# Performance work log

Measured on AMD Instinct MI355X. Metric: run time of the kernel, lower is better.

The kernel has to match this reference:

```python
import jax, jax.numpy as jnp
import numpy as np

HIDDEN = 2048
HEADS = 16
HEAD_DIM = HIDDEN // HEADS


def setup_inputs() -> dict:
    key = jax.random.key(0)
    ks = jax.random.split(key, 9)
    s = 1.0 / np.sqrt(HIDDEN)
    return {
        "hidden_states": jax.random.normal(ks[0], (2, 2048, HIDDEN), dtype=jnp.float32),
        "wq": jax.random.uniform(ks[1], (HIDDEN, HIDDEN), jnp.float32, -s, s),
        "bq": jax.random.uniform(ks[2], (HIDDEN,), jnp.float32, -s, s),
        "wk": jax.random.uniform(ks[3], (HIDDEN, HIDDEN), jnp.float32, -s, s),
        "bk": jax.random.uniform(ks[4], (HIDDEN,), jnp.float32, -s, s),
        "wv": jax.random.uniform(ks[5], (HIDDEN, HIDDEN), jnp.float32, -s, s),
        "bv": jax.random.uniform(ks[6], (HIDDEN,), jnp.float32, -s, s),
        "wo": jax.random.uniform(ks[7], (HIDDEN, HIDDEN), jnp.float32, -s, s),
        "bo": jax.random.uniform(ks[8], (HIDDEN,), jnp.float32, -s, s),
    }


def reference(hidden_states, wq, bq, wk, bk, wv, bv, wo, bo):
    B, S, _ = hidden_states.shape
    # QKV projections (nn.Linear: x @ W^T + b)
    q = hidden_states @ wq.T + bq
    k = hidden_states @ wk.T + bk
    v = hidden_states @ wv.T + bv
    # [B, S, H, D] -> [B, H, S, D]
    q = q.reshape(B, S, HEADS, HEAD_DIM).transpose(0, 2, 1, 3)
    k = k.reshape(B, S, HEADS, HEAD_DIM).transpose(0, 2, 1, 3)
    v = v.reshape(B, S, HEADS, HEAD_DIM).transpose(0, 2, 1, 3)
    scale = HEAD_DIM ** (-0.5)
    scores = jnp.einsum("bhqd,bhkd->bhqk", q, k) * scale  # [B,H,S,S]
    attn = jax.nn.softmax(scores, axis=-1)
    out = jnp.einsum("bhqk,bhkd->bhqd", attn, v)
    out = out.transpose(0, 2, 1, 3).reshape(B, S, HIDDEN)
    return out @ wo.T + bo
```

## Files before the change

### kernel.cpp

```cpp
#include <hip/hip_runtime.h>
#include <math.h>

#define HID 2048
#define NB  2
#define SEQ 2048
#define NT  (NB*SEQ)
#define NH  16
#define HD  128

typedef __attribute__((ext_vector_type(8))) _Float16 f16x8;
typedef __attribute__((ext_vector_type(4))) float    f32x4;

#define QSCALE 0.12751742f

__device__ __forceinline__ unsigned short f2h(float x) {
    union { _Float16 h; unsigned short u; } c;
    c.h = (_Float16)x;
    return c.u;
}

extern "C" __global__ __launch_bounds__(256)
void cast_x(const float* __restrict__ src, unsigned short* __restrict__ dst, int n4)
{
    const int i = blockIdx.x * 256 + threadIdx.x;
    if (i >= n4) return;
    const float4 x = ((const float4*)src)[i];
    ushort4 h;
    h.x = f2h(x.x); h.y = f2h(x.y); h.z = f2h(x.z); h.w = f2h(x.w);
    ((ushort4*)dst)[i] = h;
}

extern "C" __global__ __launch_bounds__(256)
void cast_w4(const float* __restrict__ s0, const float* __restrict__ s1,
             const float* __restrict__ s2, const float* __restrict__ s3,
             unsigned short* __restrict__ d0, unsigned short* __restrict__ d1,
             unsigned short* __restrict__ d2, unsigned short* __restrict__ d3,
             int n4)
{
    const int which = blockIdx.y;
    const float* __restrict__ src =
        (which==0) ? s0 : (which==1) ? s1 : (which==2) ? s2 : s3;
    unsigned short* __restrict__ dst =
        (which==0) ? d0 : (which==1) ? d1 : (which==2) ? d2 : d3;
    const int i = blockIdx.x * 256 + threadIdx.x;
    if (i >= n4) return;
    const float4 x = ((const float4*)src)[i];
    ushort4 h;
    h.x = f2h(x.x); h.y = f2h(x.y); h.z = f2h(x.z); h.w = f2h(x.w);
    ((ushort4*)dst)[i] = h;
}

extern "C" __global__ __launch_bounds__(256)
void qkv_f16(const unsigned short* __restrict__ Xh,
             const unsigned short* __restrict__ Wqh,
             const unsigned short* __restrict__ Wkh,
             const unsigned short* __restrict__ Wvh,
             const float* __restrict__ bq, const float* __restrict__ bk,
             const float* __restrict__ bv,
             unsigned short* __restrict__ Qb, unsigned short* __restrict__ Kb,
             unsigned short* __restrict__ Vb)
{
    const int on0 = blockIdx.x * 128;
    const int tm0 = blockIdx.y * 128;
    const int which = blockIdx.z;
    const unsigned short* __restrict__ W = (which==0) ? Wqh : (which==1) ? Wkh : Wvh;
    const float* __restrict__ bias      = (which==0) ? bq  : (which==1) ? bk  : bv;

    __shared__ unsigned short Ah[8192], Bh[8192];

    const int tid  = threadIdx.x;
    const int lane = tid & 63;
    const int w    = tid >> 6;
    const int wm   = (w & 1) * 64;
    const int wn   = (w >> 1) * 64;
    const int fr   = lane & 15;
    const int quad = lane >> 4;

    f32x4 acc[4][4];
    #pragma unroll
    for (int i = 0; i < 4; ++i)
        #pragma unroll
        for (int j = 0; j < 4; ++j)
            acc[i][j] = (f32x4){0.f, 0.f, 0.f, 0.f};

    for (int kb = 0; kb < HID/64; ++kb) {
        __syncthreads();
        const unsigned short* Asrc = Xh + (size_t)tm0*HID + kb*64;
        const unsigned short* Bsrc = W  + (size_t)on0*HID + kb*64;
        #pragma unroll
        for (int r = 0; r < 4; ++r) {
            const int p   = (r*4 + w)*64 + lane;
            const int row = p >> 3;
            const int c   = (p & 7) ^ (row & 7);
            __builtin_amdgcn_global_load_lds(
                (const __attribute__((address_space(1))) void*)(Asrc + (size_t)row*HID + c*8),
                (__attribute__((address_space(3))) void*)(Ah + (r*4 + w)*512), 16, 0, 0);
            __builtin_amdgcn_global_load_lds(
                (const __attribute__((address_space(1))) void*)(Bsrc + (size_t)row*HID + c*8),
                (__attribute__((address_space(3))) void*)(Bh + (r*4 + w)*512), 16, 0, 0);
        }
        __syncthreads();

        #pragma unroll
        for (int kk = 0; kk < 2; ++kk) {
            f16x8 a[4], b[4];
            #pragma unroll
            for (int i = 0; i < 4; ++i) {
                const int ra = wm + i*16 + fr;
                a[i] = *(const f16x8*)(Ah + (ra*8 + ((kk*4 + quad) ^ (ra & 7)))*8);
                const int rb = wn + i*16 + fr;
                b[i] = *(const f16x8*)(Bh + (rb*8 + ((kk*4 + quad) ^ (rb & 7)))*8);
            }
            #pragma unroll
            for (int i = 0; i < 4; ++i)
                #pragma unroll
                for (int j = 0; j < 4; ++j)
                    acc[i][j] = __builtin_amdgcn_mfma_f32_16x16x32_f16(a[i], b[j], acc[i][j], 0, 0, 0);
        }
    }

    const int col_l = fr;
    if (which == 2) {
        #pragma unroll
        for (int j = 0; j < 4; ++j) {
            const int o = on0 + wn + j*16 + col_l;
            const float bb = bias[o];
            const int h = o >> 7, d = o & (HD-1);
            #pragma unroll
            for (int i = 0; i < 4; ++i)
                #pragma unroll
                for (int rg = 0; rg < 4; ++rg) {
                    const int t = tm0 + wm + i*16 + quad*4 + rg;
                    const int b = t >> 11, s = t & (SEQ-1);
                    const int pos = (s & ~63) | (((s & 15) << 2) | ((s >> 4) & 3));
                    Vb[((size_t)(b*NH + h)*HD + d)*SEQ + pos] = f2h(acc[i][j][rg] + bb);
                }
        }
    } else {
        const float sc = (which == 0) ? QSCALE : 1.0f;
        unsigned short* __restrict__ dstp = (which == 0) ? Qb : Kb;
        #pragma unroll
        for (int j = 0; j < 4; ++j) {
            const int o = on0 + wn + j*16 + col_l;
            const float bb = bias[o];
            const int h = o >> 7, d = o & (HD-1);
            #pragma unroll
            for (int i = 0; i < 4; ++i)
                #pragma unroll
                for (int rg = 0; rg < 4; ++rg) {
                    const int t = tm0 + wm + i*16 + quad*4 + rg;
                    const int b = t >> 11, s = t & (SEQ-1);
                    dstp[((size_t)(b*NH + h)*SEQ + s)*HD + d] =
                        f2h((acc[i][j][rg] + bb) * sc);
                }
        }
    }
}

#define PS_STRIDE 72

extern "C" __global__ __launch_bounds__(256)
void attn_mfma(const unsigned short* __restrict__ Qg, const unsigned short* __restrict__ Kg,
               const unsigned short* __restrict__ Vtg, unsigned short* __restrict__ Of)
{
    const int L  = blockIdx.x;
    const int q0 = (L >> 5) * 128;
    const int bh = ((L & 7) << 2) | ((L >> 3) & 3);
    const unsigned short* __restrict__ Qp = Qg  + (size_t)bh * SEQ * HD;
    const unsigned short* __restrict__ Kp = Kg  + (size_t)bh * SEQ * HD;
    const unsigned short* __restrict__ Vp = Vtg + (size_t)bh * HD * SEQ;

    __shared__ alignas(16) unsigned short Ks[64*128];
    __shared__ alignas(16) unsigned short Vts[128*64];
    __shared__ alignas(16) unsigned short Ps[4][32*PS_STRIDE];

    const int tid  = threadIdx.x;
    const int lane = tid & 63;
    const int w    = tid >> 6;
    const int fr   = lane & 15;
    const int quad = lane >> 4;

    f16x8 qf[2][4];
    #pragma unroll
    for (int m16 = 0; m16 < 2; ++m16)
        #pragma unroll
        for (int c = 0; c < 4; ++c)
            qf[m16][c] = *(const f16x8*)(Qp + (size_t)(q0 + w*32 + m16*16 + fr)*HD
                                            + c*32 + quad*8);

    f32x4 accO[2][8];
    #pragma unroll
    for (int m16 = 0; m16 < 2; ++m16)
        #pragma unroll
        for (int n = 0; n < 8; ++n)
            accO[m16][n] = (f32x4){0.f, 0.f, 0.f, 0.f};
    float lp[2][4] = {};

    for (int kt = 0; kt < SEQ/64; ++kt) {
        __syncthreads();
        {
            const unsigned short* Kt = Kp + (size_t)kt*64*HD;
            #pragma unroll
            for (int r = 0; r < 4; ++r) {
                const int p   = (r*4 + w)*64 + lane;
                const int row = p >> 4;
                const int c   = (p & 15) ^ (row & 15);
                __builtin_amdgcn_global_load_lds(
                    (const __attribute__((address_space(1))) void*)(Kt + (size_t)row*HD + c*8),
                    (__attribute__((address_space(3))) void*)(Ks + (r*4 + w)*512), 16, 0, 0);
            }
            #pragma unroll
            for (int r = 0; r < 4; ++r) {
                const int p   = (r*4 + w)*64 + lane;
                const int row = p >> 3;
                const int c   = (p & 7) ^ (row & 7);
                __builtin_amdgcn_global_load_lds(
                    (const __attribute__((address_space(1))) void*)(Vp + (size_t)row*SEQ + kt*64 + c*8),
                    (__attribute__((address_space(3))) void*)(Vts + (r*4 + w)*512), 16, 0, 0);
            }
        }
        __syncthreads();

        f32x4 accS[2][4];
        #pragma unroll
        for (int m16 = 0; m16 < 2; ++m16)
            #pragma unroll
            for (int n = 0; n < 4; ++n)
                accS[m16][n] = (f32x4){0.f, 0.f, 0.f, 0.f};
        #pragma unroll
        for (int c = 0; c < 4; ++c) {
            f16x8 bf[4];
            #pragma unroll
            for (int n = 0; n < 4; ++n)
                bf[n] = *(const f16x8*)(Ks + (n*16 + fr)*128 + ((c*4 + quad) ^ fr)*8);
            #pragma unroll
            for (int m16 = 0; m16 < 2; ++m16)
                #pragma unroll
                for (int n = 0; n < 4; ++n)
                    accS[m16][n] = __builtin_amdgcn_mfma_f32_16x16x32_f16(
                        qf[m16][c], bf[n], accS[m16][n], 0, 0, 0);
        }

        #pragma unroll
        for (int m16 = 0; m16 < 2; ++m16)
            #pragma unroll
            for (int rg = 0; rg < 4; ++rg) {
                float p0 = exp2f(accS[m16][0][rg]);
                float p1 = exp2f(accS[m16][1][rg]);
                float p2 = exp2f(accS[m16][2][rg]);
                float p3 = exp2f(accS[m16][3][rg]);
                lp[m16][rg] += (p0 + p1) + (p2 + p3);
                ushort4 st;
                st.x = f2h(p0); st.y = f2h(p1); st.z = f2h(p2); st.w = f2h(p3);
                *(ushort4*)(&Ps[w][(m16*16 + quad*4 + rg)*PS_STRIDE + fr*4]) = st;
            }

        #pragma unroll
        for (int cc = 0; cc < 2; ++cc) {
            f16x8 pf[2], vf[8];
            #pragma unroll
            for (int m16 = 0; m16 < 2; ++m16)
                pf[m16] = *(const f16x8*)(&Ps[w][(m16*16 + fr)*PS_STRIDE + cc*32 + quad*8]);
            #pragma unroll
            for (int n = 0; n < 8; ++n)
                vf[n] = *(const f16x8*)(Vts + (n*16 + fr)*64 + ((cc*4 + quad) ^ (fr & 7))*8);
            #pragma unroll
            for (int m16 = 0; m16 < 2; ++m16)
                #pragma unroll
                for (int n = 0; n < 8; ++n)
                    accO[m16][n] = __builtin_amdgcn_mfma_f32_16x16x32_f16(
                        pf[m16], vf[n], accO[m16][n], 0, 0, 0);
        }
    }

    #pragma unroll
    for (int m16 = 0; m16 < 2; ++m16) {
        float inv[4];
        #pragma unroll
        for (int rg = 0; rg < 4; ++rg) {
            float l = lp[m16][rg];
            l += __shfl_xor(l, 1);
            l += __shfl_xor(l, 2);
            l += __shfl_xor(l, 4);
            l += __shfl_xor(l, 8);
            inv[rg] = 1.0f / l;
        }
        #pragma unroll
        for (int n = 0; n < 8; ++n) {
            const int d = n*16 + fr;
            #pragma unroll
            for (int rg = 0; rg < 4; ++rg) {
                const int s = q0 + w*32 + m16*16 + quad*4 + rg;
                Of[((size_t)bh*SEQ + s)*HD + d] = f2h(accO[m16][n][rg] * inv[rg]);
            }
        }
    }
}

extern "C" __global__ __launch_bounds__(256)
void oproj_f16(const unsigned short* __restrict__ Af,
               const unsigned short* __restrict__ Woh,
               const float* __restrict__ bo, float* __restrict__ Y)
{
    const int on0 = blockIdx.x * 128;
    const int tm0 = blockIdx.y * 128;

    __shared__ unsigned short Ah[8192], Bh[8192];

    const int tid  = threadIdx.x;
    const int lane = tid & 63;
    const int w    = tid >> 6;
    const int wm   = (w & 1) * 64;
    const int wn   = (w >> 1) * 64;
    const int fr   = lane & 15;
    const int quad = lane >> 4;

    f32x4 acc[4][4];
    #pragma unroll
    for (int i = 0; i < 4; ++i)
        #pragma unroll
        for (int j = 0; j < 4; ++j)
            acc[i][j] = (f32x4){0.f, 0.f, 0.f, 0.f};

    for (int kb = 0; kb < HID/64; ++kb) {
        const int hh  = kb >> 1;
        const int dd0 = (kb & 1) * 64;
        __syncthreads();
        const unsigned short* Bsrc = Woh + (size_t)on0*HID + kb*64;
        #pragma unroll
        for (int r = 0; r < 4; ++r) {
            const int p   = (r*4 + w)*64 + lane;
            const int row = p >> 3;
            const int c   = (p & 7) ^ (row & 7);
            const int t = tm0 + row, b = t >> 11, s = t & (SEQ-1);
            __builtin_amdgcn_global_load_lds(
                (const __attribute__((address_space(1))) void*)
                    (Af + ((size_t)(b*NH + hh)*SEQ + s)*HD + dd0 + c*8),
                (__attribute__((address_space(3))) void*)(Ah + (r*4 + w)*512), 16, 0, 0);
            __builtin_amdgcn_global_load_lds(
                (const __attribute__((address_space(1))) void*)(Bsrc + (size_t)row*HID + c*8),
                (__attribute__((address_space(3))) void*)(Bh + (r*4 + w)*512), 16, 0, 0);
        }
        __syncthreads();

        #pragma unroll
        for (int kk = 0; kk < 2; ++kk) {
            f16x8 a[4], b[4];
            #pragma unroll
            for (int i = 0; i < 4; ++i) {
                const int ra = wm + i*16 + fr;
                a[i] = *(const f16x8*)(Ah + (ra*8 + ((kk*4 + quad) ^ (ra & 7)))*8);
                const int rb = wn + i*16 + fr;
                b[i] = *(const f16x8*)(Bh + (rb*8 + ((kk*4 + quad) ^ (rb & 7)))*8);
            }
            #pragma unroll
            for (int i = 0; i < 4; ++i)
                #pragma unroll
                for (int j = 0; j < 4; ++j)
                    acc[i][j] = __builtin_amdgcn_mfma_f32_16x16x32_f16(a[i], b[j], acc[i][j], 0, 0, 0);
        }
    }

    const int col_l = fr;
    #pragma unroll
    for (int j = 0; j < 4; ++j) {
        const int o = on0 + wn + j*16 + col_l;
        const float bb = bo[o];
        #pragma unroll
        for (int i = 0; i < 4; ++i)
            #pragma unroll
            for (int rg = 0; rg < 4; ++rg) {
                const int t = tm0 + wm + i*16 + quad*4 + rg;
                Y[(size_t)t*HID + o] = acc[i][j][rg] + bb;
            }
    }
}

extern "C" void kernel_launch(void* const* d_in, const int* in_sizes, int n_in,
                              void* d_out, int out_size, void* d_ws, size_t ws_size,
                              hipStream_t stream)
{
    const float* X  = (const float*)d_in[0];
    const float* wq = (const float*)d_in[1];
    const float* bq = (const float*)d_in[2];
    const float* wk = (const float*)d_in[3];
    const float* bk = (const float*)d_in[4];
    const float* wv = (const float*)d_in[5];
    const float* bv = (const float*)d_in[6];
    const float* wo = (const float*)d_in[7];
    const float* bo = (const float*)d_in[8];
    float* Y = (float*)d_out;

    const size_t F  = (size_t)NT * HID;
    const size_t Wn = (size_t)HID * HID;

    unsigned short* Qb  = (unsigned short*)d_ws;
    unsigned short* Kb  = Qb  + F;
    unsigned short* Vb  = Kb  + F;
    unsigned short* Of  = Vb  + F;
    unsigned short* Xh  = Of  + F;
    unsigned short* Wqh = Xh  + F;
    unsigned short* Wkh = Wqh + Wn;
    unsigned short* Wvh = Wkh + Wn;
    unsigned short* Woh = Wvh + Wn;

    cast_x<<<(int)(F/4/256), 256, 0, stream>>>(X, Xh, (int)(F/4));
    cast_w4<<<dim3((int)(Wn/4/256), 4), 256, 0, stream>>>(
        wq, wk, wv, wo, Wqh, Wkh, Wvh, Woh, (int)(Wn/4));

    qkv_f16<<<dim3(HID/128, NT/128, 3), 256, 0, stream>>>(
        Xh, Wqh, Wkh, Wvh, bq, bk, bv, Qb, Kb, Vb);

    attn_mfma<<<dim3(512, 1, 1), 256, 0, stream>>>(Qb, Kb, Vb, Of);

    oproj_f16<<<dim3(HID/128, NT/128), 256, 0, stream>>>(Of, Woh, bo, Y);
}
```

Before: 454.8 us.

## Split attention block across eight waves of 16 query rows each

```diff
diff --git a/kernel.cpp b/kernel.cpp
--- a/kernel.cpp
+++ b/kernel.cpp
@@ -9,6 +9,7 @@
 #define HD  128
 
 typedef __attribute__((ext_vector_type(8))) _Float16 f16x8;
+typedef __attribute__((ext_vector_type(2))) __fp16   h16x2;
 typedef __attribute__((ext_vector_type(4))) float    f32x4;
 
 #define QSCALE 0.12751742f
@@ -159,7 +160,7 @@
 
 #define PS_STRIDE 72
 
-extern "C" __global__ __launch_bounds__(256)
+extern "C" __global__ __launch_bounds__(512, 4)
 void attn_mfma(const unsigned short* __restrict__ Qg, const unsigned short* __restrict__ Kg,
                const unsigned short* __restrict__ Vtg, unsigned short* __restrict__ Of)
 {
@@ -172,7 +173,7 @@
 
     __shared__ alignas(16) unsigned short Ks[64*128];
     __shared__ alignas(16) unsigned short Vts[128*64];
-    __shared__ alignas(16) unsigned short Ps[4][32*PS_STRIDE];
+    __shared__ alignas(16) unsigned short Ps[8][16*PS_STRIDE];
 
     const int tid  = threadIdx.x;
     const int lane = tid & 63;
@@ -180,119 +181,106 @@
     const int fr   = lane & 15;
     const int quad = lane >> 4;
 
-    f16x8 qf[2][4];
-    #pragma unroll
-    for (int m16 = 0; m16 < 2; ++m16)
-        #pragma unroll
-        for (int c = 0; c < 4; ++c)
-            qf[m16][c] = *(const f16x8*)(Qp + (size_t)(q0 + w*32 + m16*16 + fr)*HD
-                                            + c*32 + quad*8);
-
-    f32x4 accO[2][8];
-    #pragma unroll
-    for (int m16 = 0; m16 < 2; ++m16)
-        #pragma unroll
-        for (int n = 0; n < 8; ++n)
-            accO[m16][n] = (f32x4){0.f, 0.f, 0.f, 0.f};
-    float lp[2][4] = {};
+    f16x8 qf[4];
+    #pragma unroll
+    for (int c = 0; c < 4; ++c)
+        qf[c] = *(const f16x8*)(Qp + (size_t)(q0 + w*16 + fr)*HD + c*32 + quad*8);
+
+    f32x4 accO[8];
+    #pragma unroll
+    for (int n = 0; n < 8; ++n)
+        accO[n] = (f32x4){0.f, 0.f, 0.f, 0.f};
+    float lp[4] = {};
 
     for (int kt = 0; kt < SEQ/64; ++kt) {
         __syncthreads();
         {
             const unsigned short* Kt = Kp + (size_t)kt*64*HD;
             #pragma unroll
-            for (int r = 0; r < 4; ++r) {
-                const int p   = (r*4 + w)*64 + lane;
+            for (int r = 0; r < 2; ++r) {
+                const int p   = (r*8 + w)*64 + lane;
                 const int row = p >> 4;
                 const int c   = (p & 15) ^ (row & 15);
                 __builtin_amdgcn_global_load_lds(
                     (const __attribute__((address_space(1))) void*)(Kt + (size_t)row*HD + c*8),
-                    (__attribute__((address_space(3))) void*)(Ks + (r*4 + w)*512), 16, 0, 0);
+                    (__attribute__((address_space(3))) void*)(Ks + (r*8 + w)*512), 16, 0, 0);
             }
             #pragma unroll
-            for (int r = 0; r < 4; ++r) {
-                const int p   = (r*4 + w)*64 + lane;
+            for (int r = 0; r < 2; ++r) {
+                const int p   = (r*8 + w)*64 + lane;
                 const int row = p >> 3;
                 const int c   = (p & 7) ^ (row & 7);
                 __builtin_amdgcn_global_load_lds(
                     (const __attribute__((address_space(1))) void*)(Vp + (size_t)row*SEQ + kt*64 + c*8),
-                    (__attribute__((address_space(3))) void*)(Vts + (r*4 + w)*512), 16, 0, 0);
+                    (__attribute__((address_space(3))) void*)(Vts + (r*8 + w)*512), 16, 0, 0);
             }
         }
         __syncthreads();
 
-        f32x4 accS[2][4];
-        #pragma unroll
-        for (int m16 = 0; m16 < 2; ++m16)
-            #pragma unroll
-            for (int n = 0; n < 4; ++n)
-                accS[m16][n] = (f32x4){0.f, 0.f, 0.f, 0.f};
+        f32x4 accS[4];
+        #pragma unroll
+        for (int n = 0; n < 4; ++n)
+            accS[n] = (f32x4){0.f, 0.f, 0.f, 0.f};
         #pragma unroll
         for (int c = 0; c < 4; ++c) {
             f16x8 bf[4];
             #pragma unroll
             for (int n = 0; n < 4; ++n)
                 bf[n] = *(const f16x8*)(Ks + (n*16 + fr)*128 + ((c*4 + quad) ^ fr)*8);
-            #pragma unroll
-            for (int m16 = 0; m16 < 2; ++m16)
-                #pragma unroll
-                for (int n = 0; n < 4; ++n)
-                    accS[m16][n] = __builtin_amdgcn_mfma_f32_16x16x32_f16(
-                        qf[m16][c], bf[n], accS[m16][n], 0, 0, 0);
-        }
-
-        #pragma unroll
-        for (int m16 = 0; m16 < 2; ++m16)
-            #pragma unroll
-            for (int rg = 0; rg < 4; ++rg) {
-                float p0 = exp2f(accS[m16][0][rg]);
-                float p1 = exp2f(accS[m16][1][rg]);
-                float p2 = exp2f(accS[m16][2][rg]);
-                float p3 = exp2f(accS[m16][3][rg]);
-                lp[m16][rg] += (p0 + p1) + (p2 + p3);
-                ushort4 st;
-                st.x = f2h(p0); st.y = f2h(p1); st.z = f2h(p2); st.w = f2h(p3);
-                *(ushort4*)(&Ps[w][(m16*16 + quad*4 + rg)*PS_STRIDE + fr*4]) = st;
-            }
+            __builtin_amdgcn_s_setprio(1);
+            #pragma unroll
+            for (int n = 0; n < 4; ++n)
+                accS[n] = __builtin_amdgcn_mfma_f32_16x16x32_f16(
+                    qf[c], bf[n], accS[n], 0, 0, 0);
+            __builtin_amdgcn_s_setprio(0);
+        }
+
+        #pragma unroll
+        for (int rg = 0; rg < 4; ++rg) {
+            float p0 = exp2f(accS[0][rg]);
+            float p1 = exp2f(accS[1][rg]);
+            float p2 = exp2f(accS[2][rg]);
+            float p3 = exp2f(accS[3][rg]);
+            lp[rg] += (p0 + p1) + (p2 + p3);
+            union { h16x2 h[2]; ushort4 u4; } pk;
+            pk.h[0] = __builtin_amdgcn_cvt_pkrtz(p0, p1);
+            pk.h[1] = __builtin_amdgcn_cvt_pkrtz(p2, p3);
+            *(ushort4*)(&Ps[w][(quad*4 + rg)*PS_STRIDE + fr*4]) = pk.u4;
+        }
 
         #pragma unroll
         for (int cc = 0; cc < 2; ++cc) {
-            f16x8 pf[2], vf[8];
-            #pragma unroll
-            for (int m16 = 0; m16 < 2; ++m16)
-                pf[m16] = *(const f16x8*)(&Ps[w][(m16*16 + fr)*PS_STRIDE + cc*32 + quad*8]);
+            f16x8 pf = *(const f16x8*)(&Ps[w][fr*PS_STRIDE + cc*32 + quad*8]);
+            f16x8 vf[8];
             #pragma unroll
             for (int n = 0; n < 8; ++n)
                 vf[n] = *(const f16x8*)(Vts + (n*16 + fr)*64 + ((cc*4 + quad) ^ (fr & 7))*8);
-            #pragma unroll
-            for (int m16 = 0; m16 < 2; ++m16)
-                #pragma unroll
-                for (int n = 0; n < 8; ++n)
-                    accO[m16][n] = __builtin_amdgcn_mfma_f32_16x16x32_f16(
-                        pf[m16], vf[n], accO[m16][n], 0, 0, 0);
-        }
-    }
-
-    #pragma unroll
-    for (int m16 = 0; m16 < 2; ++m16) {
-        float inv[4];
+            __builtin_amdgcn_s_setprio(1);
+            #pragma unroll
+            for (int n = 0; n < 8; ++n)
+                accO[n] = __builtin_amdgcn_mfma_f32_16x16x32_f16(
+                    pf, vf[n], accO[n], 0, 0, 0);
+            __builtin_amdgcn_s_setprio(0);
+        }
+    }
+
+    float inv[4];
+    #pragma unroll
+    for (int rg = 0; rg < 4; ++rg) {
+        float l = lp[rg];
+        l += __shfl_xor(l, 1);
+        l += __shfl_xor(l, 2);
+        l += __shfl_xor(l, 4);
+        l += __shfl_xor(l, 8);
+        inv[rg] = 1.0f / l;
+    }
+    #pragma unroll
+    for (int n = 0; n < 8; ++n) {
+        const int d = n*16 + fr;
         #pragma unroll
         for (int rg = 0; rg < 4; ++rg) {
-            float l = lp[m16][rg];
-            l += __shfl_xor(l, 1);
-            l += __shfl_xor(l, 2);
-            l += __shfl_xor(l, 4);
-            l += __shfl_xor(l, 8);
-            inv[rg] = 1.0f / l;
-        }
-        #pragma unroll
-        for (int n = 0; n < 8; ++n) {
-            const int d = n*16 + fr;
-            #pragma unroll
-            for (int rg = 0; rg < 4; ++rg) {
-                const int s = q0 + w*32 + m16*16 + quad*4 + rg;
-                Of[((size_t)bh*SEQ + s)*HD + d] = f2h(accO[m16][n][rg] * inv[rg]);
-            }
+            const int s = q0 + w*16 + quad*4 + rg;
+            Of[((size_t)bh*SEQ + s)*HD + d] = f2h(accO[n][rg] * inv[rg]);
         }
     }
 }
@@ -411,7 +399,7 @@
     qkv_f16<<<dim3(HID/128, NT/128, 3), 256, 0, stream>>>(
         Xh, Wqh, Wkh, Wvh, bq, bk, bv, Qb, Kb, Vb);
 
-    attn_mfma<<<dim3(512, 1, 1), 256, 0, stream>>>(Qb, Kb, Vb, Of);
+    attn_mfma<<<dim3(512, 1, 1), 512, 0, stream>>>(Qb, Kb, Vb, Of);
 
     oproj_f16<<<dim3(HID/128, NT/128), 256, 0, stream>>>(Of, Woh, bo, Y);
 }
```

Result: faster. 413.3 us (-9.1%).
